# Kernel tuning notes

Measured on AMD Instinct MI355X. Metric: run time of the kernel, lower is better.

Reference implementation:

```python
import jax, jax.numpy as jnp
import numpy as np

EMBED_DIM = 64
NUM_ITEM = 1000000
BATCH = 131072
SEQ_LEN = 5
# fixed_arc = "AND,0,~1;OR,2,3;AND,5,6;OR,~7,4" parsed: (module, (pos, negated), (pos, negated))
ARC = [("AND", (0, False), (1, True)),
       ("OR",  (2, False), (3, False)),
       ("AND", (5, False), (6, False)),
       ("OR",  (7, True),  (4, False))]


def setup_inputs() -> dict:
    key = jax.random.key(0)
    ks = jax.random.split(key, 20)
    std = 0.01  # init_params: normal(0, 0.01)
    inp = {}
    inp["seq"] = jax.random.randint(ks[0], (BATCH, SEQ_LEN), 0, NUM_ITEM, dtype=jnp.int32)
    inp["pos_target"] = jax.random.randint(ks[1], (BATCH,), 0, NUM_ITEM, dtype=jnp.int32)
    inp["neg_target"] = jax.random.randint(ks[2], (BATCH,), 0, NUM_ITEM, dtype=jnp.int32)
    inp["item_embed"] = std * jax.random.normal(ks[3], (NUM_ITEM, EMBED_DIM), dtype=jnp.float32)
    t = jax.random.uniform(ks[4], (EMBED_DIM,), minval=0.0, maxval=0.1, dtype=jnp.float32)
    inp["true_vec"] = t / jnp.maximum(jnp.linalg.norm(t), 1e-12)
    inp["not_W1"] = std * jax.random.normal(ks[5], (EMBED_DIM, EMBED_DIM), dtype=jnp.float32)
    inp["not_b1"] = std * jax.random.normal(ks[6], (EMBED_DIM,), dtype=jnp.float32)
    inp["not_W2"] = std * jax.random.normal(ks[7], (EMBED_DIM, EMBED_DIM), dtype=jnp.float32)
    inp["not_b2"] = std * jax.random.normal(ks[8], (EMBED_DIM,), dtype=jnp.float32)
    inp["and_W1"] = std * jax.random.normal(ks[9], (2 * EMBED_DIM, EMBED_DIM), dtype=jnp.float32)
    inp["and_b1"] = std * jax.random.normal(ks[10], (EMBED_DIM,), dtype=jnp.float32)
    inp["and_W2"] = std * jax.random.normal(ks[11], (EMBED_DIM, EMBED_DIM), dtype=jnp.float32)
    inp["and_b2"] = std * jax.random.normal(ks[12], (EMBED_DIM,), dtype=jnp.float32)
    inp["or_W1"] = std * jax.random.normal(ks[13], (2 * EMBED_DIM, EMBED_DIM), dtype=jnp.float32)
    inp["or_b1"] = std * jax.random.normal(ks[14], (EMBED_DIM,), dtype=jnp.float32)
    inp["or_W2"] = std * jax.random.normal(ks[15], (EMBED_DIM, EMBED_DIM), dtype=jnp.float32)
    inp["or_b2"] = std * jax.random.normal(ks[16], (EMBED_DIM,), dtype=jnp.float32)
    return inp


def _mlp(x, W1, b1, W2, b2):
    # _get_ln_module(num_layers=2, dropout=0): Linear -> LeakyReLU -> Dropout(0) -> Linear
    h = jax.nn.leaky_relu(x @ W1 + b1, negative_slope=0.01)
    return h @ W2 + b2


def reference(seq, pos_target, neg_target, item_embed, true_vec,
              not_W1, not_b1, not_W2, not_b2,
              and_W1, and_b1, and_W2, and_b2,
              or_W1, or_b1, or_W2, or_b2):
    NOT = lambda x: _mlp(x, not_W1, not_b1, not_W2, not_b2)
    AND = lambda x: _mlp(x, and_W1, and_b1, and_W2, and_b2)
    OR = lambda x: _mlp(x, or_W1, or_b1, or_W2, or_b2)
    mods = {"AND": AND, "OR": OR}

    intermediates = {}

    def get_input(pos, neg):
        if pos < SEQ_LEN:
            e = item_embed[seq[:, pos]]  # [B, D] embedding gather
        else:
            e = intermediates[pos]
        return NOT(e) if neg else e

    out = None
    for layer_id, (name, (p1, n1), (p2, n2)) in enumerate(ARC):
        i1 = get_input(p1, n1)
        i2 = get_input(p2, n2)
        out = mods[name](jnp.concatenate((i1, i2), axis=-1))
        intermediates[SEQ_LEN + layer_id] = out

    enc_not = NOT(out)  # [B, D]
    pos_e = item_embed[pos_target]
    neg_e = item_embed[neg_target]
    encoded_pos = OR(jnp.concatenate((enc_not, pos_e), axis=-1))
    encoded_neg = OR(jnp.concatenate((enc_not, neg_e), axis=-1))
    encoded = jnp.concatenate((encoded_pos, encoded_neg), axis=0)  # [2B, D]

    # cosine similarity vs 'true' anchor, amplified by 10 (cos_amplify_factor)
    eps = 1e-8
    num = encoded @ true_vec
    denom = jnp.maximum(jnp.linalg.norm(encoded, axis=-1), eps) * jnp.maximum(jnp.linalg.norm(true_vec), eps)
    prediction = (num / denom) * 10.0
    return prediction
```

## Files before the change

### kernel.cpp

```cpp
#include <hip/hip_runtime.h>
#include <stdint.h>
#include <math.h>

#define BATCH 131072
#define WS_TN_OFF 65536
#define WS_B_OFF  65544

typedef __attribute__((ext_vector_type(8)))  short short8;
typedef __attribute__((ext_vector_type(16))) float float16;
typedef __attribute__((ext_vector_type(2)))  unsigned int uint2v;

union S8 { short8 s; uint32_t u[4]; };
union F8 { float f[8]; uint32_t u[8]; float4 v4[2]; };

__global__ __launch_bounds__(256)
void prep_kernel(const float* __restrict__ tvec,
                 const float* __restrict__ nW1, const float* __restrict__ nW2,
                 const float* __restrict__ aW1, const float* __restrict__ aW2,
                 const float* __restrict__ oW1, const float* __restrict__ oW2,
                 const float* __restrict__ nb1, const float* __restrict__ nb2,
                 const float* __restrict__ ab1, const float* __restrict__ ab2,
                 const float* __restrict__ ob1, const float* __restrict__ ob2,
                 char* __restrict__ ws)
{
    const int id = blockIdx.x * 256 + threadIdx.x;
    if (id == 0) {
        float s = 0.f;
        for (int j = 0; j < 64; ++j) s = fmaf(tvec[j], tvec[j], s);
        *(float*)(ws + WS_TN_OFF) = fmaxf(sqrtf(s), 1e-8f);
    }
    if (id < 32768) {
        const float* srcs[8] = { nW1, nW2, aW1, aW1 + 4096, aW2, oW1, oW1 + 4096, oW2 };
        const int u    = id >> 12;
        const int e    = id & 4095;
        const int j    = e & 7;
        const int lane = (e >> 3) & 63;
        const int f    = e >> 9;
        const int nt   = f & 1, kc = f >> 1;
        const int k    = kc * 16 + (lane >> 5) * 8 + j;
        const int n    = nt * 32 + (lane & 31);
        const uint32_t b = __float_as_uint(srcs[u][k * 64 + n]);
        const uint32_t r = b + 0x7fffu + ((b >> 16) & 1u);
        ((uint16_t*)(ws + u * 8192 + f * 1024 + lane * 16))[j] = (uint16_t)(r >> 16);
    } else if (id < 33152) {
        const int b   = id - 32768;
        const int arr = b >> 6, j = b & 63;
        const float* bp = (arr == 0) ? nb1 : (arr == 1) ? nb2 : (arr == 2) ? ab1
                        : (arr == 3) ? ab2 : (arr == 4) ? ob1 : ob2;
        ((float*)(ws + WS_B_OFF))[b] = bp[j];
    } else if (id < 33216) {
        const int j = id - 33152;
        ((float*)(ws + WS_B_OFF + 1536))[j] = tvec[j];
    }
}

#define OPW(g,u,sH,ini,bid,ep,rd,sl,pg) \
    ((g)|((u)<<3)|((sH)<<6)|((ini)<<7)|((bid)<<8)|((ep)<<11)|((rd)<<13)|((sl)<<15)|((pg)<<16))

__global__ __launch_bounds__(256, 3)
void logicnet_mfma(const int* __restrict__ seq, const int* __restrict__ post,
                   const int* __restrict__ negt, const float* __restrict__ E,
                   const char* __restrict__ ws, float* __restrict__ out)
{
    static const uint32_t PROG[24] = {
        OPW(0,5,0,1,4,0,0,0,0),
        OPW(1,6,0,0,0,1,0,0,2),
        OPW(0,7,0,1,5,3,0,0,0),
        OPW(1,0,0,1,0,1,0,0,1),
        OPW(0,1,0,1,1,2,0,0,0),
        OPW(0,3,0,1,2,0,0,0,0),
        OPW(1,2,0,0,0,1,0,0,0),
        OPW(0,4,0,1,3,2,0,0,0),
        OPW(0,2,0,1,2,0,0,0,0),
        OPW(0,3,1,0,0,1,0,0,0),
        OPW(0,4,0,1,3,2,0,0,0),
        OPW(0,0,0,1,0,1,0,0,5),
        OPW(0,1,0,1,1,2,0,0,0),
        OPW(0,5,0,1,4,0,0,0,0),
        OPW(1,6,0,0,0,1,0,0,0),
        OPW(0,7,0,1,5,2,0,0,0),
        OPW(0,0,0,1,0,1,0,0,6),
        OPW(0,1,0,1,1,3,0,1,0),
        OPW(0,5,1,1,4,0,0,1,0),
        OPW(1,6,0,0,0,1,0,0,7),
        OPW(0,7,0,1,5,0,1,0,0),
        OPW(0,5,1,1,4,0,0,1,0),
        OPW(1,6,0,0,0,1,0,0,0),
        OPW(0,7,0,1,5,0,2,0,0),
    };

    __shared__ uint32_t lds[448 + 4096 + 4096];
    const int tid  = threadIdx.x;
    const int wid  = tid >> 6;
    const int lane = tid & 63;
    const int m    = lane & 31;
    const int h    = lane >> 5;
    const int rowbase = (blockIdx.x * 4 + wid) * 32;
    const int rr   = rowbase + m;

    uint32_t* const slot0 = &lds[448 + wid * 1024];
    uint32_t* const slot1 = &lds[448 + 4096 + wid * 1024];
    const float* const ldsb = (const float*)lds;
    const float* const ltv  = (const float*)(lds + 384);

    const int sv0 = seq[(size_t)rr * 5 + 0], sv1 = seq[(size_t)rr * 5 + 1];
    const int sv2 = seq[(size_t)rr * 5 + 2], sv3 = seq[(size_t)rr * 5 + 3];
    const int sv4 = seq[(size_t)rr * 5 + 4];
    const int ipv = post[rr], imv = negt[rr];

    float16 acc[2];
    S8 xhi[4], xlo[4];
    F8 gx[4];
    float tn;

    auto gissue = [&](int idx) {
        const float4* e = (const float4*)(E + (size_t)idx * 64 + h * 8);
#pragma unroll
        for (int kc = 0; kc < 4; ++kc) { gx[kc].v4[0] = e[kc * 4]; gx[kc].v4[1] = e[kc * 4 + 1]; }
    };
    auto gpack = [&]() {
#pragma unroll
        for (int kc = 0; kc < 4; ++kc) {
#pragma unroll
            for (int w = 0; w < 4; ++w) {
                const uint32_t b0 = gx[kc].u[2 * w], b1 = gx[kc].u[2 * w + 1];
                xhi[kc].u[w] = __builtin_amdgcn_perm(b1, b0, 0x07060302u);
                const float l0 = gx[kc].f[2 * w]     - __uint_as_float(b0 & 0xffff0000u);
                const float l1 = gx[kc].f[2 * w + 1] - __uint_as_float(b1 & 0xffff0000u);
                xlo[kc].u[w] = __builtin_amdgcn_perm(__float_as_uint(l1), __float_as_uint(l0), 0x07060302u);
            }
        }
    };

    auto uaP = [&](int u) {
        const char* wb = ws + u * 8192 + lane * 16;
#pragma unroll
        for (int kc = 0; kc < 4; ++kc) {
            const short8 w0 = *(const short8*)(wb + (kc * 2 + 0) * 1024);
            const short8 w1 = *(const short8*)(wb + (kc * 2 + 1) * 1024);
            acc[0] = __builtin_amdgcn_mfma_f32_32x32x16_bf16(w0, xhi[kc].s, acc[0], 0, 0, 0);
            acc[1] = __builtin_amdgcn_mfma_f32_32x32x16_bf16(w1, xhi[kc].s, acc[1], 0, 0, 0);
            acc[0] = __builtin_amdgcn_mfma_f32_32x32x16_bf16(w0, xlo[kc].s, acc[0], 0, 0, 0);
            acc[1] = __builtin_amdgcn_mfma_f32_32x32x16_bf16(w1, xlo[kc].s, acc[1], 0, 0, 0);
        }
    };

    auto uaH = [&](int u, const uint32_t* slot) {
        const char* wb = ws + u * 8192 + lane * 16;
#pragma unroll
        for (int kc = 0; kc < 4; ++kc) {
            const short8 xf = *(const short8*)(slot + kc * 256 + lane * 4);
            const short8 w0 = *(const short8*)(wb + (kc * 2 + 0) * 1024);
            const short8 w1 = *(const short8*)(wb + (kc * 2 + 1) * 1024);
            acc[0] = __builtin_amdgcn_mfma_f32_32x32x16_bf16(w0, xf, acc[0], 0, 0, 0);
            acc[1] = __builtin_amdgcn_mfma_f32_32x32x16_bf16(w1, xf, acc[1], 0, 0, 0);
        }
    };

    auto epiX = [&](bool act) {
#pragma unroll
        for (int nt = 0; nt < 2; ++nt) {
#pragma unroll
            for (int c = 0; c < 2; ++c) {
                uint32_t ph[2][2], pl[2][2];
#pragma unroll
                for (int d = 0; d < 2; ++d) {
                    const int g2 = 2 * c + d;
                    float v0 = acc[nt][4 * g2 + 0], v1 = acc[nt][4 * g2 + 1];
                    float v2 = acc[nt][4 * g2 + 2], v3 = acc[nt][4 * g2 + 3];
                    if (act) {
                        v0 = fmaxf(v0, 0.01f * v0); v1 = fmaxf(v1, 0.01f * v1);
                        v2 = fmaxf(v2, 0.01f * v2); v3 = fmaxf(v3, 0.01f * v3);
                    }
                    const uint32_t b0 = __float_as_uint(v0), b1 = __float_as_uint(v1);
                    const uint32_t b2 = __float_as_uint(v2), b3 = __float_as_uint(v3);
                    ph[d][0] = __builtin_amdgcn_perm(b1, b0, 0x07060302u);
                    ph[d][1] = __builtin_amdgcn_perm(b3, b2, 0x07060302u);
                    const float l0 = v0 - __uint_as_float(b0 & 0xffff0000u);
                    const float l1 = v1 - __uint_as_float(b1 & 0xffff0000u);
                    const float l2 = v2 - __uint_as_float(b2 & 0xffff0000u);
                    const float l3 = v3 - __uint_as_float(b3 & 0xffff0000u);
                    pl[d][0] = __builtin_amdgcn_perm(__float_as_uint(l1), __float_as_uint(l0), 0x07060302u);
                    pl[d][1] = __builtin_amdgcn_perm(__float_as_uint(l3), __float_as_uint(l2), 0x07060302u);
                }
                const int kc = 2 * nt + c;
#pragma unroll
                for (int w = 0; w < 2; ++w) {
                    uint2v rh = __builtin_amdgcn_permlane32_swap(ph[0][w], ph[1][w], false, false);
                    xhi[kc].u[w]     = rh[0];
                    xhi[kc].u[2 + w] = rh[1];
                    uint2v rl = __builtin_amdgcn_permlane32_swap(pl[0][w], pl[1][w], false, false);
                    xlo[kc].u[w]     = rl[0];
                    xlo[kc].u[2 + w] = rl[1];
                }
            }
        }
    };

    auto epiB = [&](uint32_t* slot) {
#pragma unroll
        for (int nt = 0; nt < 2; ++nt) {
#pragma unroll
            for (int c = 0; c < 2; ++c) {
                uint32_t pp[2][2];
#pragma unroll
                for (int d = 0; d < 2; ++d) {
                    const int g2 = 2 * c + d;
                    asm("v_cvt_pk_bf16_f32 %0, %1, %2"
                        : "=v"(pp[d][0]) : "v"(acc[nt][4 * g2 + 0]), "v"(acc[nt][4 * g2 + 1]));
                    asm("v_cvt_pk_bf16_f32 %0, %1, %2"
                        : "=v"(pp[d][1]) : "v"(acc[nt][4 * g2 + 2]), "v"(acc[nt][4 * g2 + 3]));
                }
                const int kc = 2 * nt + c;
                S8 o;
#pragma unroll
                for (int w = 0; w < 2; ++w) {
                    uint2v r = __builtin_amdgcn_permlane32_swap(pp[0][w], pp[1][w], false, false);
                    o.u[w]     = r[0];
                    o.u[2 + w] = r[1];
                }
                *(short8*)(slot + kc * 256 + lane * 4) = o.s;
            }
        }
    };

    auto reduce = [&](float* outp) {
        float num = 0.f, ss = 0.f;
#pragma unroll
        for (int nt = 0; nt < 2; ++nt)
#pragma unroll
            for (int g2 = 0; g2 < 4; ++g2) {
                const float4 t4 = *(const float4*)(ltv + nt * 32 + g2 * 8 + h * 4);
                const float y0 = acc[nt][4 * g2 + 0], y1 = acc[nt][4 * g2 + 1];
                const float y2 = acc[nt][4 * g2 + 2], y3 = acc[nt][4 * g2 + 3];
                num = fmaf(y0, t4.x, fmaf(y1, t4.y, fmaf(y2, t4.z, fmaf(y3, t4.w, num))));
                ss  = fmaf(y0, y0, fmaf(y1, y1, fmaf(y2, y2, fmaf(y3, y3, ss))));
            }
        num += __shfl_xor(num, 32, 64);
        ss  += __shfl_xor(ss, 32, 64);
        if (h == 0) outp[m] = num / (fmaxf(sqrtf(ss), 1e-8f) * tn) * 10.0f;
    };

    for (int t = tid; t < 448; t += 256) lds[t] = ((const uint32_t*)(ws + WS_B_OFF))[t];
    gissue(sv2);
    __syncthreads();
    tn = *(const float*)(ws + WS_TN_OFF);
    gpack();
    gissue(sv3);

#pragma unroll 1
    for (int op = 0; op < 24; ++op) {
        const uint32_t cw = PROG[op];
        const int g   = cw & 7;
        const int u   = (cw >> 3) & 7;
        const int sH  = (cw >> 6) & 1;
        const int ini = (cw >> 7) & 1;
        const int bid = (cw >> 8) & 7;
        const int ep  = (cw >> 11) & 3;
        const int rd  = (cw >> 13) & 3;
        const int sl  = (cw >> 15) & 1;
        const int pg  = (cw >> 16) & 7;

        if (g) gpack();

        if (ini) {
#pragma unroll
            for (int nt = 0; nt < 2; ++nt)
#pragma unroll
                for (int g2 = 0; g2 < 4; ++g2) {
                    const float4 b4 = *(const float4*)(ldsb + bid * 64 + nt * 32 + g2 * 8 + h * 4);
                    acc[nt][4 * g2 + 0] = b4.x; acc[nt][4 * g2 + 1] = b4.y;
                    acc[nt][4 * g2 + 2] = b4.z; acc[nt][4 * g2 + 3] = b4.w;
                }
        }

        __builtin_amdgcn_s_setprio(1);
        if (sH) uaH(u, sl ? slot1 : slot0);
        else    uaP(u);
        __builtin_amdgcn_s_setprio(0);

        if (pg) {
            int idx;
            switch (pg) {
                case 1: idx = sv0; break;
                case 2: idx = sv1; break;
                case 3: idx = sv2; break;
                case 4: idx = sv3; break;
                case 5: idx = sv4; break;
                case 6: idx = ipv; break;
                default: idx = imv; break;
            }
            gissue(idx);
        }

        if (ep == 1)      epiX(true);
        else if (ep == 2) epiX(false);
        else if (ep == 3) epiB(sl ? slot1 : slot0);

        if (rd == 1)      reduce(out + rowbase);
        else if (rd == 2) reduce(out + BATCH + rowbase);
    }
}

extern "C" void kernel_launch(void* const* d_in, const int* in_sizes, int n_in,
                              void* d_out, int out_size, void* d_ws, size_t ws_size,
                              hipStream_t stream) {
    const int*   seq  = (const int*)  d_in[0];
    const int*   post = (const int*)  d_in[1];
    const int*   negt = (const int*)  d_in[2];
    const float* E    = (const float*)d_in[3];
    const float* tv   = (const float*)d_in[4];
    const float* nW1  = (const float*)d_in[5];
    const float* nb1  = (const float*)d_in[6];
    const float* nW2  = (const float*)d_in[7];
    const float* nb2  = (const float*)d_in[8];
    const float* aW1  = (const float*)d_in[9];
    const float* ab1  = (const float*)d_in[10];
    const float* aW2  = (const float*)d_in[11];
    const float* ab2  = (const float*)d_in[12];
    const float* oW1  = (const float*)d_in[13];
    const float* ob1  = (const float*)d_in[14];
    const float* oW2  = (const float*)d_in[15];
    const float* ob2  = (const float*)d_in[16];
    float* out = (float*)d_out;
    char*  ws  = (char*)d_ws;

    hipLaunchKernelGGL(prep_kernel, dim3(130), dim3(256), 0, stream,
                       tv, nW1, nW2, aW1, aW2, oW1, oW2,
                       nb1, nb2, ab1, ab2, ob1, ob2, ws);
    hipLaunchKernelGGL(logicnet_mfma, dim3(BATCH / 128), dim3(256), 0, stream,
                       seq, post, negt, E, ws, out);
}
```

Baseline: 481.8 us.

## Move low-half bf16 operands to LDS and drop gather prefetch to raise occupancy

The low bf16 split of the activations now lives in LDS instead of registers. The software-prefetched gather buffer is removed, so each embedding row is loaded and packed just in time before use. Together these free VGPRs, and launch bounds go from 3 to 4 waves per EU. The cost is exposed gather latency, since the gather is no longer overlapped with the previous MFMA block, plus extra LDS traffic for the low operands. The second LDS slot is repurposed for the low halves, so the two-slot saved-input scheme is removed, which looks valid given the program ordering.

```diff
diff --git a/kernel.cpp b/kernel.cpp
--- a/kernel.cpp
+++ b/kernel.cpp
@@ -54,39 +54,39 @@
     }
 }
 
-#define OPW(g,u,sH,ini,bid,ep,rd,sl,pg) \
-    ((g)|((u)<<3)|((sH)<<6)|((ini)<<7)|((bid)<<8)|((ep)<<11)|((rd)<<13)|((sl)<<15)|((pg)<<16))
-
-__global__ __launch_bounds__(256, 3)
+#define OPW(g,u,sH,ini,bid,ep,rd) \
+    ((g)|((u)<<3)|((sH)<<6)|((ini)<<7)|((bid)<<8)|((ep)<<11)|((rd)<<13))
+
+__global__ __launch_bounds__(256, 4)
 void logicnet_mfma(const int* __restrict__ seq, const int* __restrict__ post,
                    const int* __restrict__ negt, const float* __restrict__ E,
                    const char* __restrict__ ws, float* __restrict__ out)
 {
     static const uint32_t PROG[24] = {
-        OPW(0,5,0,1,4,0,0,0,0),
-        OPW(1,6,0,0,0,1,0,0,2),
-        OPW(0,7,0,1,5,3,0,0,0),
-        OPW(1,0,0,1,0,1,0,0,1),
-        OPW(0,1,0,1,1,2,0,0,0),
-        OPW(0,3,0,1,2,0,0,0,0),
-        OPW(1,2,0,0,0,1,0,0,0),
-        OPW(0,4,0,1,3,2,0,0,0),
-        OPW(0,2,0,1,2,0,0,0,0),
-        OPW(0,3,1,0,0,1,0,0,0),
-        OPW(0,4,0,1,3,2,0,0,0),
-        OPW(0,0,0,1,0,1,0,0,5),
-        OPW(0,1,0,1,1,2,0,0,0),
-        OPW(0,5,0,1,4,0,0,0,0),
-        OPW(1,6,0,0,0,1,0,0,0),
-        OPW(0,7,0,1,5,2,0,0,0),
-        OPW(0,0,0,1,0,1,0,0,6),
-        OPW(0,1,0,1,1,3,0,1,0),
-        OPW(0,5,1,1,4,0,0,1,0),
-        OPW(1,6,0,0,0,1,0,0,7),
-        OPW(0,7,0,1,5,0,1,0,0),
-        OPW(0,5,1,1,4,0,0,1,0),
-        OPW(1,6,0,0,0,1,0,0,0),
-        OPW(0,7,0,1,5,0,2,0,0),
+        OPW(0,5,0,1,4,0,0),
+        OPW(4,6,0,0,0,1,0),
+        OPW(0,7,0,1,5,3,0),
+        OPW(2,0,0,1,0,1,0),
+        OPW(0,1,0,1,1,2,0),
+        OPW(0,3,0,1,2,0,0),
+        OPW(1,2,0,0,0,1,0),
+        OPW(0,4,0,1,3,2,0),
+        OPW(0,2,0,1,2,0,0),
+        OPW(0,3,1,0,0,1,0),
+        OPW(0,4,0,1,3,2,0),
+        OPW(0,0,0,1,0,1,0),
+        OPW(0,1,0,1,1,2,0),
+        OPW(0,5,0,1,4,0,0),
+        OPW(5,6,0,0,0,1,0),
+        OPW(0,7,0,1,5,2,0),
+        OPW(0,0,0,1,0,1,0),
+        OPW(0,1,0,1,1,3,0),
+        OPW(0,5,1,1,4,0,0),
+        OPW(6,6,0,0,0,1,0),
+        OPW(0,7,0,1,5,0,1),
+        OPW(0,5,1,1,4,0,0),
+        OPW(7,6,0,0,0,1,0),
+        OPW(0,7,0,1,5,0,2),
     };
 
     __shared__ uint32_t lds[448 + 4096 + 4096];
@@ -98,8 +98,8 @@
     const int rowbase = (blockIdx.x * 4 + wid) * 32;
     const int rr   = rowbase + m;
 
-    uint32_t* const slot0 = &lds[448 + wid * 1024];
-    uint32_t* const slot1 = &lds[448 + 4096 + wid * 1024];
+    uint32_t* const slot = &lds[448 + wid * 1024];
+    uint32_t* const xloL = &lds[448 + 4096 + wid * 1024];
     const float* const ldsb = (const float*)lds;
     const float* const ltv  = (const float*)(lds + 384);
 
@@ -109,43 +109,52 @@
     const int ipv = post[rr], imv = negt[rr];
 
     float16 acc[2];
-    S8 xhi[4], xlo[4];
-    F8 gx[4];
+    S8 xhi[4];
     float tn;
 
-    auto gissue = [&](int idx) {
+    auto packkc = [&](const F8& t, int kc) {
+        S8 lo;
+#pragma unroll
+        for (int w = 0; w < 4; ++w) {
+            const uint32_t b0 = t.u[2 * w], b1 = t.u[2 * w + 1];
+            xhi[kc].u[w] = __builtin_amdgcn_perm(b1, b0, 0x07060302u);
+            const float l0 = t.f[2 * w]     - __uint_as_float(b0 & 0xffff0000u);
+            const float l1 = t.f[2 * w + 1] - __uint_as_float(b1 & 0xffff0000u);
+            lo.u[w] = __builtin_amdgcn_perm(__float_as_uint(l1), __float_as_uint(l0), 0x07060302u);
+        }
+        *(short8*)(xloL + kc * 256 + lane * 4) = lo.s;
+    };
+
+    auto gw = [&](int idx) {
         const float4* e = (const float4*)(E + (size_t)idx * 64 + h * 8);
 #pragma unroll
-        for (int kc = 0; kc < 4; ++kc) { gx[kc].v4[0] = e[kc * 4]; gx[kc].v4[1] = e[kc * 4 + 1]; }
-    };
-    auto gpack = [&]() {
-#pragma unroll
-        for (int kc = 0; kc < 4; ++kc) {
-#pragma unroll
-            for (int w = 0; w < 4; ++w) {
-                const uint32_t b0 = gx[kc].u[2 * w], b1 = gx[kc].u[2 * w + 1];
-                xhi[kc].u[w] = __builtin_amdgcn_perm(b1, b0, 0x07060302u);
-                const float l0 = gx[kc].f[2 * w]     - __uint_as_float(b0 & 0xffff0000u);
-                const float l1 = gx[kc].f[2 * w + 1] - __uint_as_float(b1 & 0xffff0000u);
-                xlo[kc].u[w] = __builtin_amdgcn_perm(__float_as_uint(l1), __float_as_uint(l0), 0x07060302u);
-            }
+        for (int hp = 0; hp < 2; ++hp) {
+            F8 t0, t1;
+            t0.v4[0] = e[(2 * hp) * 4];     t0.v4[1] = e[(2 * hp) * 4 + 1];
+            t1.v4[0] = e[(2 * hp + 1) * 4]; t1.v4[1] = e[(2 * hp + 1) * 4 + 1];
+            packkc(t0, 2 * hp);
+            packkc(t1, 2 * hp + 1);
         }
     };
 
     auto uaP = [&](int u) {
         const char* wb = ws + u * 8192 + lane * 16;
+        S8 cur, nxt;
+        cur.s = *(const short8*)(xloL + lane * 4);
 #pragma unroll
         for (int kc = 0; kc < 4; ++kc) {
+            if (kc < 3) nxt.s = *(const short8*)(xloL + (kc + 1) * 256 + lane * 4);
             const short8 w0 = *(const short8*)(wb + (kc * 2 + 0) * 1024);
             const short8 w1 = *(const short8*)(wb + (kc * 2 + 1) * 1024);
             acc[0] = __builtin_amdgcn_mfma_f32_32x32x16_bf16(w0, xhi[kc].s, acc[0], 0, 0, 0);
             acc[1] = __builtin_amdgcn_mfma_f32_32x32x16_bf16(w1, xhi[kc].s, acc[1], 0, 0, 0);
-            acc[0] = __builtin_amdgcn_mfma_f32_32x32x16_bf16(w0, xlo[kc].s, acc[0], 0, 0, 0);
-            acc[1] = __builtin_amdgcn_mfma_f32_32x32x16_bf16(w1, xlo[kc].s, acc[1], 0, 0, 0);
-        }
-    };
-
-    auto uaH = [&](int u, const uint32_t* slot) {
+            acc[0] = __builtin_amdgcn_mfma_f32_32x32x16_bf16(w0, cur.s, acc[0], 0, 0, 0);
+            acc[1] = __builtin_amdgcn_mfma_f32_32x32x16_bf16(w1, cur.s, acc[1], 0, 0, 0);
+            cur = nxt;
+        }
+    };
+
+    auto uaH = [&](int u) {
         const char* wb = ws + u * 8192 + lane * 16;
 #pragma unroll
         for (int kc = 0; kc < 4; ++kc) {
@@ -184,20 +193,22 @@
                     pl[d][1] = __builtin_amdgcn_perm(__float_as_uint(l3), __float_as_uint(l2), 0x07060302u);
                 }
                 const int kc = 2 * nt + c;
+                S8 lo;
 #pragma unroll
                 for (int w = 0; w < 2; ++w) {
                     uint2v rh = __builtin_amdgcn_permlane32_swap(ph[0][w], ph[1][w], false, false);
                     xhi[kc].u[w]     = rh[0];
                     xhi[kc].u[2 + w] = rh[1];
                     uint2v rl = __builtin_amdgcn_permlane32_swap(pl[0][w], pl[1][w], false, false);
-                    xlo[kc].u[w]     = rl[0];
-                    xlo[kc].u[2 + w] = rl[1];
-                }
+                    lo.u[w]     = rl[0];
+                    lo.u[2 + w] = rl[1];
+                }
+                *(short8*)(xloL + kc * 256 + lane * 4) = lo.s;
             }
         }
     };
 
-    auto epiB = [&](uint32_t* slot) {
+    auto epiB = [&]() {
 #pragma unroll
         for (int nt = 0; nt < 2; ++nt) {
 #pragma unroll
@@ -242,11 +253,9 @@
     };
 
     for (int t = tid; t < 448; t += 256) lds[t] = ((const uint32_t*)(ws + WS_B_OFF))[t];
-    gissue(sv2);
+    gw(sv2);
     __syncthreads();
     tn = *(const float*)(ws + WS_TN_OFF);
-    gpack();
-    gissue(sv3);
 
 #pragma unroll 1
     for (int op = 0; op < 24; ++op) {
@@ -258,30 +267,10 @@
         const int bid = (cw >> 8) & 7;
         const int ep  = (cw >> 11) & 3;
         const int rd  = (cw >> 13) & 3;
-        const int sl  = (cw >> 15) & 1;
-        const int pg  = (cw >> 16) & 7;
-
-        if (g) gpack();
-
-        if (ini) {
-#pragma unroll
-            for (int nt = 0; nt < 2; ++nt)
-#pragma unroll
-                for (int g2 = 0; g2 < 4; ++g2) {
-                    const float4 b4 = *(const float4*)(ldsb + bid * 64 + nt * 32 + g2 * 8 + h * 4);
-                    acc[nt][4 * g2 + 0] = b4.x; acc[nt][4 * g2 + 1] = b4.y;
-                    acc[nt][4 * g2 + 2] = b4.z; acc[nt][4 * g2 + 3] = b4.w;
-                }
-        }
-
-        __builtin_amdgcn_s_setprio(1);
-        if (sH) uaH(u, sl ? slot1 : slot0);
-        else    uaP(u);
-        __builtin_amdgcn_s_setprio(0);
-
-        if (pg) {
+
+        if (g) {
             int idx;
-            switch (pg) {
+            switch (g) {
                 case 1: idx = sv0; break;
                 case 2: idx = sv1; break;
                 case 3: idx = sv2; break;
@@ -290,12 +279,28 @@
                 case 6: idx = ipv; break;
                 default: idx = imv; break;
             }
-            gissue(idx);
-        }
+            gw(idx);
+        }
+
+        if (ini) {
+#pragma unroll
+            for (int nt = 0; nt < 2; ++nt)
+#pragma unroll
+                for (int g2 = 0; g2 < 4; ++g2) {
+                    const float4 b4 = *(const float4*)(ldsb + bid * 64 + nt * 32 + g2 * 8 + h * 4);
+                    acc[nt][4 * g2 + 0] = b4.x; acc[nt][4 * g2 + 1] = b4.y;
+                    acc[nt][4 * g2 + 2] = b4.z; acc[nt][4 * g2 + 3] = b4.w;
+                }
+        }
+
+        __builtin_amdgcn_s_setprio(1);
+        if (sH) uaH(u);
+        else    uaP(u);
+        __builtin_amdgcn_s_setprio(0);
 
         if (ep == 1)      epiX(true);
         else if (ep == 2) epiX(false);
-        else if (ep == 3) epiB(sl ? slot1 : slot0);
+        else if (ep == 3) epiB();
 
         if (rd == 1)      reduce(out + rowbase);
         else if (rd == 2) reduce(out + BATCH + rowbase);
```

New measurement: 396.0 us. -17.8%, faster.
